# Kernel optimization log

Measured on AMD Instinct MI355X. Metric: run time of the kernel, lower is better.

Reference implementation:

```python
import jax, jax.numpy as jnp
import numpy as np

B, D = 8192, 1024            # batch, inputs_dim
H1, H2, H3 = 2048, 1024, 512 # expert_units
NS, NT = 8, 4                # num_shared_experts, num_tasks_experts
E = NS + 3 * NT              # 20 experts total: [shared 0:8 | SA 8:12 | RA 12:16 | EA 16:20]
TU1, TU2 = 1024, 512         # tower_units
TIN = H3 * 4                 # tower input dim = 2048


def lrelu(x):
    return jnp.where(x >= 0, x, 0.1 * x)


def setup_inputs() -> dict:
    key = jax.random.key(0)
    ks = jax.random.split(key, 24)
    s = 0.02
    return {
        "inputs": jax.random.normal(ks[0], (B, D), jnp.float32),
        # stacked expert MLP params (leading axis = expert index)
        "W1": jax.random.normal(ks[1], (E, D, H1), jnp.float32) * s,
        "b1": jnp.zeros((E, H1), jnp.float32),
        "W2": jax.random.normal(ks[2], (E, H1, H2), jnp.float32) * s,
        "b2": jnp.zeros((E, H2), jnp.float32),
        "W3": jax.random.normal(ks[3], (E, H2, H3), jnp.float32) * s,
        "b3": jnp.zeros((E, H3), jnp.float32),
        # gate linears (single layer + softmax over dim 1)
        "Wg_sh": jax.random.normal(ks[4], (D, NS + 3 * NT), jnp.float32) * s,
        "bg_sh": jnp.zeros((NS + 3 * NT,), jnp.float32),
        "Wg_sa": jax.random.normal(ks[5], (D, NT + NS), jnp.float32) * s,
        "bg_sa": jnp.zeros((NT + NS,), jnp.float32),
        "Wg_ra": jax.random.normal(ks[6], (D, NT + NS), jnp.float32) * s,
        "bg_ra": jnp.zeros((NT + NS,), jnp.float32),
        "Wg_ea": jax.random.normal(ks[7], (D, NT + NS), jnp.float32) * s,
        "bg_ea": jnp.zeros((NT + NS,), jnp.float32),
        # 2 towers (one per task), stacked on leading axis
        "Wt1": jax.random.normal(ks[8], (2, TIN, TU1), jnp.float32) * s,
        "bt1": jnp.zeros((2, TU1), jnp.float32),
        "Wt2": jax.random.normal(ks[9], (2, TU1, TU2), jnp.float32) * s,
        "bt2": jnp.zeros((2, TU2), jnp.float32),
        # per-task output denses: PRESENCE=6, AIRFLOW=4
        "Wd0": jax.random.normal(ks[10], (TU2, 6), jnp.float32) * s,
        "bd0": jnp.zeros((6,), jnp.float32),
        "Wd1": jax.random.normal(ks[11], (TU2, 4), jnp.float32) * s,
        "bd1": jnp.zeros((4,), jnp.float32),
    }


def reference(inputs, W1, b1, W2, b2, W3, b3,
              Wg_sh, bg_sh, Wg_sa, bg_sa, Wg_ra, bg_ra, Wg_ea, bg_ea,
              Wt1, bt1, Wt2, bt2, Wd0, bd0, Wd1, bd1):
    x = inputs
    # all 20 experts as batched GEMMs: [E, B, h]
    h = lrelu(jnp.einsum('bd,edh->ebh', x, W1) + b1[:, None, :])
    h = lrelu(jnp.einsum('ebh,ehk->ebk', h, W2) + b2[:, None, :])
    eo = lrelu(jnp.einsum('ebk,eko->ebo', h, W3) + b3[:, None, :])  # [E,B,H3]

    # gates (softmax over feature dim)
    g_sh = jax.nn.softmax(x @ Wg_sh + bg_sh, axis=1)  # [B, 20]
    g_sa = jax.nn.softmax(x @ Wg_sa + bg_sa, axis=1)  # [B, 12]
    g_ra = jax.nn.softmax(x @ Wg_ra + bg_ra, axis=1)
    g_ea = jax.nn.softmax(x @ Wg_ea + bg_ea, axis=1)

    # shared gate: order = shared + SA + RA + EA == natural stacking order
    out_sh = jnp.einsum('ebh,be->bh', eo, g_sh)
    # task gates: order = task experts + shared experts
    out_sa = jnp.einsum('ebh,be->bh', jnp.concatenate([eo[NS:NS+NT], eo[:NS]], 0), g_sa)
    out_ra = jnp.einsum('ebh,be->bh', jnp.concatenate([eo[NS+NT:NS+2*NT], eo[:NS]], 0), g_ra)
    out_ea = jnp.einsum('ebh,be->bh', jnp.concatenate([eo[NS+2*NT:], eo[:NS]], 0), g_ea)

    tower_in = jnp.concatenate([out_sh, out_sa, out_ra, out_ea], axis=1)  # [B, 2048]
    t = lrelu(jnp.einsum('bi,kio->kbo', tower_in, Wt1) + bt1[:, None, :])  # [2,B,TU1]
    t = lrelu(jnp.einsum('kbo,kop->kbp', t, Wt2) + bt2[:, None, :])        # [2,B,TU2]
    out0 = t[0] @ Wd0 + bd0  # [B, 6]  PRESENCE
    out1 = t[1] @ Wd1 + bd1  # [B, 4]  AIRFLOW
    return (out0, out1)
```

## Files before the change

### kernel.cpp

```cpp
#include <hip/hip_runtime.h>

#define DEV __device__ __forceinline__

typedef __bf16 bf16x8 __attribute__((ext_vector_type(8)));
typedef float f32x4 __attribute__((ext_vector_type(4)));

DEV unsigned short f2bf(float f) {
  union { float f; unsigned u; } v; v.f = f;
  unsigned r = v.u + 0x7FFFu + ((v.u >> 16) & 1u);
  return (unsigned short)(r >> 16);
}
DEV float bf2f(unsigned short h) {
  union { float f; unsigned u; } v; v.u = ((unsigned)h) << 16;
  return v.f;
}

DEV void gload16(const void* g, void* l) {
  __builtin_amdgcn_global_load_lds(
      (__attribute__((address_space(1))) void*)(g),
      (__attribute__((address_space(3))) void*)(l), 16, 0, 0);
}

#define MFMA16(a, b, c) __builtin_amdgcn_mfma_f32_16x16x32_bf16((a), (b), (c), 0, 0, 0)

__global__ __launch_bounds__(512) void gemm256(
    const unsigned short* __restrict__ A,
    const unsigned short* __restrict__ Bt,
    const float* __restrict__ bias,
    unsigned short* __restrict__ Out,
    int K, int lda, int ldo, int nbx, int nby,
    long sA, long sB, long sBias, long sOut)
{
  int wg = blockIdx.x;
  {
    const int nwg = gridDim.x;
    const int q = nwg >> 3, r = nwg & 7;
    const int xcd = wg & 7, pos = wg >> 3;
    wg = (xcd < r ? xcd * (q + 1) : r * (q + 1) + (xcd - r) * q) + pos;
  }
  const int per_z = nbx * nby;
  const int z  = wg / per_z;
  const int rz = wg - z * per_z;
  const int by = rz / nbx;
  const int bx = rz - by * nbx;

  A    += (size_t)z * sA;
  Bt   += (size_t)z * sB;
  bias += (size_t)z * sBias;
  Out  += (size_t)z * sOut;

  const int tid  = threadIdx.x;
  const int lane = tid & 63;
  const int wid  = tid >> 6;
  const int wm   = wid >> 2, wn = wid & 3;
  const int m0   = by * 256, n0 = bx * 256;

  __shared__ alignas(16) char sm[2][65536];

  f32x4 acc[8][4];
  const f32x4 fz = {0.f, 0.f, 0.f, 0.f};
#pragma unroll
  for (int i = 0; i < 8; ++i)
#pragma unroll
    for (int j = 0; j < 4; ++j) acc[i][j] = fz;

  const int rr = tid >> 3;
  const int ch = (tid & 7) ^ (rr & 7);
  const char* gA = (const char*)A  + ((size_t)(m0 + rr) * lda) * 2 + ch * 16;
  const char* gB = (const char*)Bt + ((size_t)(n0 + rr) * K)   * 2 + ch * 16;
  const size_t stepA = (size_t)64 * lda * 2;
  const size_t stepB = (size_t)64 * K * 2;

  const int koff0 = (((lane >> 4) << 4) ^ ((lane & 7) << 4));
  const int aRow  = wm * 128 + (lane & 15);
  const int bRow  = wn * 64  + (lane & 15);

  const int nkt = K >> 6;

  auto SA = [&](int buf, int kt, int jh) {
    const char* s = gA + (size_t)kt * 128 + (2 * jh) * stepA;
    char* l = sm[buf] + tid * 16 + (2 * jh) * 8192;
    gload16(s, l);
    gload16(s + stepA, l + 8192);
  };
  auto SB = [&](int buf, int kt, int jh) {
    const char* s = gB + (size_t)kt * 128 + (2 * jh) * stepB;
    char* l = sm[buf] + 32768 + tid * 16 + (2 * jh) * 8192;
    gload16(s, l);
    gload16(s + stepB, l + 8192);
  };

  SA(0, 0, 0); SA(0, 0, 1); SB(0, 0, 0); SB(0, 0, 1);

  for (int kt = 0; kt < nkt; ++kt) {
    const int cur = kt & 1, nb = cur ^ 1;
    const bool pre = (kt + 1 < nkt);
    if (pre) {
      SA(nb, kt + 1, 0);
      asm volatile("s_waitcnt vmcnt(2)" ::: "memory");
    } else {
      asm volatile("s_waitcnt vmcnt(0)" ::: "memory");
    }
    __builtin_amdgcn_s_barrier();
    __builtin_amdgcn_sched_barrier(0);

    const char* pA = sm[cur] + aRow * 128;
    const char* pB = sm[cur] + 32768 + bRow * 128;
    bf16x8 a0[4], a1[4], b0[4], b1[4];

    {
#pragma unroll
      for (int i = 0; i < 4; ++i) a0[i] = *(const bf16x8*)(pA + i * 2048 + koff0);
#pragma unroll
      for (int n = 0; n < 4; ++n) b0[n] = *(const bf16x8*)(pB + n * 2048 + koff0);
      if (pre) SA(nb, kt + 1, 1);
      asm volatile("s_waitcnt lgkmcnt(0)" ::: "memory");
      __builtin_amdgcn_sched_barrier(0);
      __builtin_amdgcn_s_setprio(1);
#pragma unroll
      for (int i = 0; i < 4; ++i)
#pragma unroll
        for (int n = 0; n < 4; ++n) acc[i][n] = MFMA16(a0[i], b0[n], acc[i][n]);
      __builtin_amdgcn_s_setprio(0);
      __builtin_amdgcn_sched_barrier(0);
      __builtin_amdgcn_s_barrier();
      __builtin_amdgcn_sched_barrier(0);
    }
    {
#pragma unroll
      for (int i = 0; i < 4; ++i) a1[i] = *(const bf16x8*)(pA + (i + 4) * 2048 + koff0);
      if (pre) { SB(nb, kt + 1, 0); SB(nb, kt + 1, 1); }
      asm volatile("s_waitcnt lgkmcnt(0)" ::: "memory");
      __builtin_amdgcn_sched_barrier(0);
      __builtin_amdgcn_s_setprio(1);
#pragma unroll
      for (int i = 0; i < 4; ++i)
#pragma unroll
        for (int n = 0; n < 4; ++n) acc[i + 4][n] = MFMA16(a1[i], b0[n], acc[i + 4][n]);
      __builtin_amdgcn_s_setprio(0);
      __builtin_amdgcn_sched_barrier(0);
      __builtin_amdgcn_s_barrier();
      __builtin_amdgcn_sched_barrier(0);
    }
    {
      const int ko = koff0 ^ 64;
#pragma unroll
      for (int i = 0; i < 4; ++i) a0[i] = *(const bf16x8*)(pA + i * 2048 + ko);
#pragma unroll
      for (int n = 0; n < 4; ++n) b1[n] = *(const bf16x8*)(pB + n * 2048 + ko);
      asm volatile("s_waitcnt lgkmcnt(0)" ::: "memory");
      __builtin_amdgcn_sched_barrier(0);
      __builtin_amdgcn_s_setprio(1);
#pragma unroll
      for (int i = 0; i < 4; ++i)
#pragma unroll
        for (int n = 0; n < 4; ++n) acc[i][n] = MFMA16(a0[i], b1[n], acc[i][n]);
      __builtin_amdgcn_s_setprio(0);
      __builtin_amdgcn_sched_barrier(0);
      __builtin_amdgcn_s_barrier();
      __builtin_amdgcn_sched_barrier(0);
    }
    {
      const int ko = koff0 ^ 64;
#pragma unroll
      for (int i = 0; i < 4; ++i) a1[i] = *(const bf16x8*)(pA + (i + 4) * 2048 + ko);
      asm volatile("s_waitcnt lgkmcnt(0)" ::: "memory");
      __builtin_amdgcn_sched_barrier(0);
      __builtin_amdgcn_s_setprio(1);
#pragma unroll
      for (int i = 0; i < 4; ++i)
#pragma unroll
        for (int n = 0; n < 4; ++n) acc[i + 4][n] = MFMA16(a1[i], b1[n], acc[i + 4][n]);
      __builtin_amdgcn_s_setprio(0);
      __builtin_amdgcn_sched_barrier(0);
      __builtin_amdgcn_s_barrier();
      __builtin_amdgcn_sched_barrier(0);
    }
  }

#pragma unroll
  for (int ni = 0; ni < 4; ++ni) {
    const int c = n0 + wn * 64 + ni * 16 + (lane & 15);
    const float bv = bias[c];
#pragma unroll
    for (int mi = 0; mi < 8; ++mi) {
      const int r0 = m0 + wm * 128 + mi * 16 + ((lane >> 4) << 2);
#pragma unroll
      for (int j = 0; j < 4; ++j) {
        float v = acc[mi][ni][j] + bv;
        v = v >= 0.f ? v : 0.1f * v;
        Out[(size_t)(r0 + j) * ldo + c] = f2bf(v);
      }
    }
  }
}

DEV float gateW(const float* Wsh, const float* Wsa, const float* Wra,
                const float* Wea, int k, int c) {
  if (c < 20) return Wsh[(size_t)k * 20 + c];
  if (c < 32) return Wsa[(size_t)k * 12 + (c - 20)];
  if (c < 44) return Wra[(size_t)k * 12 + (c - 32)];
  if (c < 56) return Wea[(size_t)k * 12 + (c - 44)];
  return 0.f;
}
DEV float gateB(const float* bsh, const float* bsa, const float* bra,
                const float* bea, int c) {
  if (c < 20) return bsh[c];
  if (c < 32) return bsa[c - 20];
  if (c < 44) return bra[c - 32];
  if (c < 56) return bea[c - 44];
  return 0.f;
}

__global__ __launch_bounds__(256) void prep_all(
    const float* __restrict__ W1,  const float* __restrict__ W2,
    const float* __restrict__ W3,  const float* __restrict__ Wt1,
    const float* __restrict__ Wt2, const float* __restrict__ x,
    const float* __restrict__ Wsh, const float* __restrict__ bsh,
    const float* __restrict__ Wsa, const float* __restrict__ bsa,
    const float* __restrict__ Wra, const float* __restrict__ bra,
    const float* __restrict__ Wea, const float* __restrict__ bea,
    unsigned short* __restrict__ W1t,  unsigned short* __restrict__ W2t,
    unsigned short* __restrict__ W3t,  unsigned short* __restrict__ Wt1t,
    unsigned short* __restrict__ Wt2t, unsigned short* __restrict__ xb,
    float* __restrict__ logits)
{
  __shared__ alignas(16) char smem[16384];
  const int id = blockIdx.x;
  const int t  = threadIdx.x;

  if (id < 128) {
    float (*sx)[64] = (float (*)[64])smem;
    float (*sw)[64] = (float (*)[64])(smem + 8192);
    const int b0 = id * 64;
    const int tr = t >> 4, tc = t & 15;
    float acc[4][4] = {};

    for (int kt = 0; kt < 32; ++kt) {
      const int k0 = kt * 32;
      __syncthreads();
#pragma unroll
      for (int it = 0; it < 2; ++it) {
        const int idx = t + it * 256;
        const int r = idx >> 3, c4 = (idx & 7) * 4;
        const float4 v = *(const float4*)(x + (size_t)(b0 + r) * 1024 + k0 + c4);
        sx[c4 + 0][r] = v.x; sx[c4 + 1][r] = v.y;
        sx[c4 + 2][r] = v.z; sx[c4 + 3][r] = v.w;
      }
#pragma unroll
      for (int it = 0; it < 2; ++it) {
        const int idx = t + it * 256;
        const int row = idx >> 4;
        const int c4  = (idx & 15) * 4;
#pragma unroll
        for (int j = 0; j < 4; ++j)
          sw[row][c4 + j] = gateW(Wsh, Wsa, Wra, Wea, k0 + row, c4 + j);
      }
      __syncthreads();
#pragma unroll
      for (int kk = 0; kk < 32; ++kk) {
        const float4 rx = *(const float4*)&sx[kk][tr * 4];
        const float4 wv = *(const float4*)&sw[kk][tc * 4];
#pragma unroll
        for (int i = 0; i < 4; ++i) {
          const float xv = (i == 0) ? rx.x : (i == 1) ? rx.y : (i == 2) ? rx.z : rx.w;
          acc[i][0] += xv * wv.x; acc[i][1] += xv * wv.y;
          acc[i][2] += xv * wv.z; acc[i][3] += xv * wv.w;
        }
      }
    }
    float bv[4];
#pragma unroll
    for (int j = 0; j < 4; ++j) bv[j] = gateB(bsh, bsa, bra, bea, tc * 4 + j);
#pragma unroll
    for (int i = 0; i < 4; ++i) {
      float4 o;
      o.x = acc[i][0] + bv[0]; o.y = acc[i][1] + bv[1];
      o.z = acc[i][2] + bv[2]; o.w = acc[i][3] + bv[3];
      *(float4*)&logits[(size_t)(b0 + tr * 4 + i) * 64 + tc * 4] = o;
    }
    return;
  }

  if (id >= 24448) {
    const int local = id - 24448;
    const int r0 = (local >> 4) * 64, c0 = (local & 15) * 64;
#pragma unroll
    for (int i = 0; i < 4; ++i) {
      const int row = r0 + i * 16 + (t >> 4);
      const int col = c0 + (t & 15) * 4;
      const float4 v = *(const float4*)(x + (size_t)row * 1024 + col);
      ushort4 u = make_ushort4(f2bf(v.x), f2bf(v.y), f2bf(v.z), f2bf(v.w));
      *(ushort4*)(xb + (size_t)row * 1024 + col) = u;
    }
    return;
  }

  const int wid2 = id - 128;
  const float* src; unsigned short* dst; int K, N, local;
  if (wid2 < 10240)      { src = W1;  dst = W1t;  K = 1024; N = 2048; local = wid2; }
  else if (wid2 < 20480) { src = W2;  dst = W2t;  K = 2048; N = 1024; local = wid2 - 10240; }
  else if (wid2 < 23040) { src = W3;  dst = W3t;  K = 1024; N = 512;  local = wid2 - 20480; }
  else if (wid2 < 24064) { src = Wt1; dst = Wt1t; K = 2048; N = 1024; local = wid2 - 23040; }
  else                   { src = Wt2; dst = Wt2t; K = 1024; N = 512;  local = wid2 - 24064; }

  const int nkt = K >> 6, nnt = N >> 6;
  const int per_z = nkt * nnt;
  const int z   = local / per_z;
  const int rem = local - z * per_z;
  const int k0  = (rem % nkt) * 64;
  const int n0  = (rem / nkt) * 64;
  src += (size_t)z * K * N;
  dst += (size_t)z * K * N;

  unsigned short (*lds)[68] = (unsigned short (*)[68])smem;
  const int cr = t >> 4;
  const int cc = (t & 15) * 4;
#pragma unroll
  for (int i = 0; i < 4; ++i) {
    const int row = i * 16 + cr;
    const float4 v = *(const float4*)(src + (size_t)(k0 + row) * N + n0 + cc);
    lds[row][cc + 0] = f2bf(v.x); lds[row][cc + 1] = f2bf(v.y);
    lds[row][cc + 2] = f2bf(v.z); lds[row][cc + 3] = f2bf(v.w);
  }
  __syncthreads();
#pragma unroll
  for (int i = 0; i < 4; ++i) {
    const int nrow = i * 16 + cr;
    ushort4 u = make_ushort4(lds[cc + 0][nrow], lds[cc + 1][nrow],
                             lds[cc + 2][nrow], lds[cc + 3][nrow]);
    *(ushort4*)(dst + (size_t)(n0 + nrow) * K + k0 + cc) = u;
  }
}

__global__ __launch_bounds__(256) void combine_k(
    const unsigned short* __restrict__ eo,
    const float* __restrict__ logits,
    unsigned short* __restrict__ tin)
{
  const int b = blockIdx.x;
  const int t = threadIdx.x;
  __shared__ alignas(16) unsigned short lds[20][512];
  __shared__ float gsm[56];
  const unsigned short* er = eo + (size_t)b * 10240;
  unsigned short* ldsf = &lds[0][0];
#pragma unroll
  for (int i = 0; i < 5; ++i)
    gload16(er + (i * 256 + t) * 8, ldsf + (i * 256 + t) * 8);

  if (t < 64) {
    const float v0 = (t < 56) ? logits[(size_t)b * 64 + t] : 0.f;
    const int off[4] = {0, 20, 32, 44};
    const int wd[4]  = {20, 12, 12, 12};
    for (int g = 0; g < 4; ++g) {
      const bool in = (t >= off[g]) && (t < off[g] + wd[g]);
      float vv = in ? v0 : -1e30f;
      float m = vv;
#pragma unroll
      for (int o = 32; o; o >>= 1) m = fmaxf(m, __shfl_xor(m, o));
      float e = in ? __expf(vv - m) : 0.f;
      float s = e;
#pragma unroll
      for (int o = 32; o; o >>= 1) s += __shfl_xor(s, o);
      if (in) gsm[t] = e / s;
    }
  }
  __syncthreads();

  const int sec = t >> 6;
  const int h0 = (t & 63) * 8;
  float acc[8] = {0.f, 0.f, 0.f, 0.f, 0.f, 0.f, 0.f, 0.f};
  if (sec == 0) {
    for (int e = 0; e < 20; ++e) {
      const float w = gsm[e];
#pragma unroll
      for (int j = 0; j < 8; ++j) acc[j] += w * bf2f(lds[e][h0 + j]);
    }
  } else {
    const int goff = 20 + (sec - 1) * 12;
    const int ebase = 8 + (sec - 1) * 4;
    for (int tt = 0; tt < 4; ++tt) {
      const float w = gsm[goff + tt];
#pragma unroll
      for (int j = 0; j < 8; ++j) acc[j] += w * bf2f(lds[ebase + tt][h0 + j]);
    }
    for (int ss = 0; ss < 8; ++ss) {
      const float w = gsm[goff + 4 + ss];
#pragma unroll
      for (int j = 0; j < 8; ++j) acc[j] += w * bf2f(lds[ss][h0 + j]);
    }
  }
  unsigned short* ob = tin + (size_t)b * 2048 + sec * 512 + h0;
  ushort4 u0 = make_ushort4(f2bf(acc[0]), f2bf(acc[1]), f2bf(acc[2]), f2bf(acc[3]));
  ushort4 u1 = make_ushort4(f2bf(acc[4]), f2bf(acc[5]), f2bf(acc[6]), f2bf(acc[7]));
  *(ushort4*)ob = u0;
  *(ushort4*)(ob + 4) = u1;
}

__global__ __launch_bounds__(256) void outd_k(
    const unsigned short* __restrict__ t2,
    const float* __restrict__ Wd0, const float* __restrict__ bd0,
    const float* __restrict__ Wd1, const float* __restrict__ bd1,
    float* __restrict__ out)
{
  const int gid = blockIdx.x * 4 + (threadIdx.x >> 6);
  const int lane = threadIdx.x & 63;
  const int b = gid >> 1, task = gid & 1;
  const uint4 raw = *(const uint4*)(t2 + ((size_t)task * 8192 + b) * 512 + lane * 8);
  const unsigned short* rs = (const unsigned short*)&raw;
  float v[8];
#pragma unroll
  for (int j = 0; j < 8; ++j) v[j] = bf2f(rs[j]);
  const float* Wd = task ? Wd1 : Wd0;
  const float* bd = task ? bd1 : bd0;
  const int ncol = task ? 4 : 6;
  float* ob = task ? (out + (size_t)8192 * 6 + (size_t)b * 4) : (out + (size_t)b * 6);
  for (int c = 0; c < ncol; ++c) {
    float p = 0.f;
#pragma unroll
    for (int j = 0; j < 8; ++j) p += v[j] * Wd[(size_t)(lane * 8 + j) * ncol + c];
#pragma unroll
    for (int o = 32; o; o >>= 1) p += __shfl_xor(p, o);
    if (lane == 0) ob[c] = p + bd[c];
  }
}

extern "C" void kernel_launch(void* const* d_in, const int* in_sizes, int n_in,
                              void* d_out, int out_size, void* d_ws, size_t ws_size,
                              hipStream_t stream) {
  const float* x     = (const float*)d_in[0];
  const float* W1    = (const float*)d_in[1];
  const float* b1    = (const float*)d_in[2];
  const float* W2    = (const float*)d_in[3];
  const float* b2    = (const float*)d_in[4];
  const float* W3    = (const float*)d_in[5];
  const float* b3    = (const float*)d_in[6];
  const float* Wg_sh = (const float*)d_in[7];
  const float* bg_sh = (const float*)d_in[8];
  const float* Wg_sa = (const float*)d_in[9];
  const float* bg_sa = (const float*)d_in[10];
  const float* Wg_ra = (const float*)d_in[11];
  const float* bg_ra = (const float*)d_in[12];
  const float* Wg_ea = (const float*)d_in[13];
  const float* bg_ea = (const float*)d_in[14];
  const float* Wt1   = (const float*)d_in[15];
  const float* bt1   = (const float*)d_in[16];
  const float* Wt2   = (const float*)d_in[17];
  const float* bt2   = (const float*)d_in[18];
  const float* Wd0   = (const float*)d_in[19];
  const float* bd0   = (const float*)d_in[20];
  const float* Wd1   = (const float*)d_in[21];
  const float* bd1   = (const float*)d_in[22];
  float* out = (float*)d_out;

  const int B = 8192, D = 1024, H1 = 2048, H2 = 1024, H3 = 512;
  const int E = 20, TU1 = 1024, TU2 = 512, TIN = 2048;

  auto rnd = [](size_t n) { return (n + 255) & ~(size_t)255; };
  const size_t szXb   = rnd((size_t)B * D * 2);
  const size_t szW1t  = rnd((size_t)E * H1 * D * 2);
  const size_t szW2t  = rnd((size_t)E * H2 * H1 * 2);
  const size_t szW3t  = rnd((size_t)E * H3 * H2 * 2);
  const size_t szWt1t = rnd((size_t)2 * TU1 * TIN * 2);
  const size_t szWt2t = rnd((size_t)2 * TU2 * TU1 * 2);
  const size_t szLog  = rnd((size_t)B * 64 * 4);
  const size_t szEo   = rnd((size_t)E * B * H3 * 2);
  const size_t szTin  = rnd((size_t)B * TIN * 2);
  const size_t szT1   = rnd((size_t)2 * B * TU1 * 2);
  const size_t szT2   = rnd((size_t)2 * B * TU2 * 2);
  const size_t szH1e  = rnd((size_t)B * H1 * 2);
  const size_t szH2e  = rnd((size_t)B * H2 * 2);
  const size_t fixed = szXb + szW1t + szW2t + szW3t + szWt1t + szWt2t +
                       szLog + szEo;
  const size_t tNeed = szTin + szT1 + szT2;

  int G = 1; bool fullh2 = false;
  {
    const int  gOpt[8]  = {20, 10, 10, 5, 5, 4, 2, 1};
    const bool fOpt[8]  = {true, true, false, true, false, false, false, false};
    for (int i = 0; i < 8; ++i) {
      const size_t h2cnt = fOpt[i] ? (size_t)E : (size_t)gOpt[i];
      size_t hNeed = (size_t)gOpt[i] * szH1e + h2cnt * szH2e;
      if (hNeed < tNeed) hNeed = tNeed;
      if (fixed + hNeed <= ws_size) { G = gOpt[i]; fullh2 = fOpt[i]; break; }
    }
  }

  char* w = (char*)d_ws;
  auto alloc = [&](size_t n) { char* p = w; w += rnd(n); return p; };
  unsigned short* xb   = (unsigned short*)alloc((size_t)B * D * 2);
  unsigned short* W1t  = (unsigned short*)alloc((size_t)E * H1 * D * 2);
  unsigned short* W2t  = (unsigned short*)alloc((size_t)E * H2 * H1 * 2);
  unsigned short* W3t  = (unsigned short*)alloc((size_t)E * H3 * H2 * 2);
  unsigned short* Wt1t = (unsigned short*)alloc((size_t)2 * TU1 * TIN * 2);
  unsigned short* Wt2t = (unsigned short*)alloc((size_t)2 * TU2 * TU1 * 2);
  float*          lgts = (float*)alloc((size_t)B * 64 * 4);
  unsigned short* eo   = (unsigned short*)alloc((size_t)E * B * H3 * 2);
  char* hreg = w;
  unsigned short* h1  = (unsigned short*)hreg;
  unsigned short* h2  = (unsigned short*)(hreg + (size_t)G * szH1e);
  unsigned short* tin = (unsigned short*)hreg;
  unsigned short* t1  = (unsigned short*)(hreg + szTin);
  unsigned short* t2  = (unsigned short*)(hreg + szTin + szT1);
  (void)in_sizes; (void)n_in; (void)out_size;

  auto launch256 = [&](const unsigned short* Ap, int lda, long sA,
                       const unsigned short* Btp, long sB,
                       const float* biasp, long sBias,
                       unsigned short* Outp, int ldo, long sOut,
                       int N, int K, int nz) {
    const int nbx = N / 256, nby = B / 256;
    gemm256<<<dim3(nbx * nby * nz), 512, 0, stream>>>(
        Ap, Btp, biasp, Outp, K, lda, ldo, nbx, nby, sA, sB, sBias, sOut);
  };

  prep_all<<<dim3(26496), 256, 0, stream>>>(
      W1, W2, W3, Wt1, Wt2, x,
      Wg_sh, bg_sh, Wg_sa, bg_sa, Wg_ra, bg_ra, Wg_ea, bg_ea,
      W1t, W2t, W3t, Wt1t, Wt2t, xb, lgts);

  for (int e0 = 0; e0 < E; e0 += G) {
    launch256(xb, D, 0,
              W1t + (size_t)e0 * H1 * D, (long)H1 * D,
              b1 + (size_t)e0 * H1, H1,
              h1, H1, (long)B * H1, H1, D, G);
    unsigned short* h2dst = fullh2 ? (h2 + (size_t)e0 * B * H2) : h2;
    launch256(h1, H1, (long)B * H1,
              W2t + (size_t)e0 * H2 * H1, (long)H2 * H1,
              b2 + (size_t)e0 * H2, H2,
              h2dst, H2, (long)B * H2, H2, H1, G);
    if (!fullh2) {
      launch256(h2, H2, (long)B * H2,
                W3t + (size_t)e0 * H3 * H2, (long)H3 * H2,
                b3 + (size_t)e0 * H3, H3,
                eo + (size_t)e0 * H3, E * H3, H3, H3, H2, G);
    }
  }
  if (fullh2) {
    launch256(h2, H2, (long)B * H2,
              W3t, (long)H3 * H2,
              b3, H3,
              eo, E * H3, H3, H3, H2, E);
  }

  combine_k<<<dim3(B), 256, 0, stream>>>(eo, lgts, tin);

  launch256(tin, TIN, 0, Wt1t, (long)TU1 * TIN, bt1, TU1,
            t1, TU1, (long)B * TU1, TU1, TIN, 2);
  launch256(t1, TU1, (long)B * TU1, Wt2t, (long)TU2 * TU1, bt2, TU2,
            t2, TU2, (long)B * TU2, TU2, TU1, 2);

  outd_k<<<dim3(B * 2 / 4), 256, 0, stream>>>(t2, Wd0, bd0, Wd1, bd1, out);
}
```

Baseline: 2.164 ms.

## Fix expert group size at two and batch layer-3 GEMMs over larger groups

The expert MLP schedule now always runs layers 1 and 2 two experts at a time. It keeps a ring of up to 10 layer-2 outputs and launches the layer-3 GEMM once per filled ring rather than per group. The aim is to keep the h1/h2 intermediates small enough to stay L2/MALL-resident while still giving layer 3 a large batched launch. The transpose prep kernel also narrows its LDS row padding and writes pairs of bf16 values with 32-bit stores instead of single 16-bit stores. The trade-off is more launches for layers 1 and 2 than the earlier large-G path, and possible bank conflicts from the changed padding.

```diff
diff --git a/kernel.cpp b/kernel.cpp
--- a/kernel.cpp
+++ b/kernel.cpp
@@ -313,15 +313,17 @@
   src += (size_t)z * K * N;
   dst += (size_t)z * K * N;
 
-  unsigned short (*lds)[68] = (unsigned short (*)[68])smem;
+  unsigned short (*lds)[66] = (unsigned short (*)[66])smem;
   const int cr = t >> 4;
   const int cc = (t & 15) * 4;
 #pragma unroll
   for (int i = 0; i < 4; ++i) {
     const int row = i * 16 + cr;
     const float4 v = *(const float4*)(src + (size_t)(k0 + row) * N + n0 + cc);
-    lds[row][cc + 0] = f2bf(v.x); lds[row][cc + 1] = f2bf(v.y);
-    lds[row][cc + 2] = f2bf(v.z); lds[row][cc + 3] = f2bf(v.w);
+    ushort2 u0; u0.x = f2bf(v.x); u0.y = f2bf(v.y);
+    ushort2 u1; u1.x = f2bf(v.z); u1.y = f2bf(v.w);
+    *(ushort2*)&lds[row][cc]     = u0;
+    *(ushort2*)&lds[row][cc + 2] = u1;
   }
   __syncthreads();
 #pragma unroll
@@ -474,15 +476,14 @@
                        szLog + szEo;
   const size_t tNeed = szTin + szT1 + szT2;
 
-  int G = 1; bool fullh2 = false;
+  const int G = 2;
+  int hg = 2;
   {
-    const int  gOpt[8]  = {20, 10, 10, 5, 5, 4, 2, 1};
-    const bool fOpt[8]  = {true, true, false, true, false, false, false, false};
-    for (int i = 0; i < 8; ++i) {
-      const size_t h2cnt = fOpt[i] ? (size_t)E : (size_t)gOpt[i];
-      size_t hNeed = (size_t)gOpt[i] * szH1e + h2cnt * szH2e;
+    const int opts[3] = {10, 5, 2};
+    for (int i = 0; i < 3; ++i) {
+      size_t hNeed = (size_t)G * szH1e + (size_t)opts[i] * szH2e;
       if (hNeed < tNeed) hNeed = tNeed;
-      if (fixed + hNeed <= ws_size) { G = gOpt[i]; fullh2 = fOpt[i]; break; }
+      if (fixed + hNeed <= ws_size) { hg = opts[i]; break; }
     }
   }
 
@@ -524,23 +525,17 @@
               W1t + (size_t)e0 * H1 * D, (long)H1 * D,
               b1 + (size_t)e0 * H1, H1,
               h1, H1, (long)B * H1, H1, D, G);
-    unsigned short* h2dst = fullh2 ? (h2 + (size_t)e0 * B * H2) : h2;
     launch256(h1, H1, (long)B * H1,
               W2t + (size_t)e0 * H2 * H1, (long)H2 * H1,
               b2 + (size_t)e0 * H2, H2,
-              h2dst, H2, (long)B * H2, H2, H1, G);
-    if (!fullh2) {
+              h2 + (size_t)(e0 % hg) * B * H2, H2, (long)B * H2, H2, H1, G);
+    if ((e0 + G) % hg == 0) {
+      const int eb = e0 + G - hg;
       launch256(h2, H2, (long)B * H2,
-                W3t + (size_t)e0 * H3 * H2, (long)H3 * H2,
-                b3 + (size_t)e0 * H3, H3,
-                eo + (size_t)e0 * H3, E * H3, H3, H3, H2, G);
-    }
-  }
-  if (fullh2) {
-    launch256(h2, H2, (long)B * H2,
-              W3t, (long)H3 * H2,
-              b3, H3,
-              eo, E * H3, H3, H3, H2, E);
+                W3t + (size_t)eb * H3 * H2, (long)H3 * H2,
+                b3 + (size_t)eb * H3, H3,
+                eo + (size_t)eb * H3, E * H3, H3, H3, H2, hg);
+    }
   }
 
   combine_k<<<dim3(B), 256, 0, stream>>>(eo, lgts, tin);
```

New measurement: 2.111 ms. -2.4%, faster.
